# Kernel optimization log

Measured on AMD Instinct MI355X. Metric: run time of the kernel, lower is better.

Reference implementation:

```python
import jax, jax.numpy as jnp
import numpy as np

POS_MARGIN = 0.01
NEG_MARGIN = 0.2
REG_WEIGHT = 0.1
N, D = 8192, 256
NUM_CLASSES = 512


def setup_inputs() -> dict:
    key = jax.random.key(0)
    k1, k2 = jax.random.split(key)
    embeds = jax.random.normal(k1, (N, D), dtype=jnp.float32)
    labels = jax.random.randint(k2, (N,), 0, NUM_CLASSES, dtype=jnp.int64)
    return {"embeds": embeds, "labels": labels}


def reference(embeds, labels):
    n, d = embeds.shape
    # L2-normalize embeddings (normalize_embeds=True)
    e = embeds / jnp.linalg.norm(embeds, axis=1, keepdims=True)

    # var(e_i - e_j, ddof=1) over feature dim, computed without the [N,N,D] tensor:
    # var = (D/(D-1)) * ( mean(e_i^2) + mean(e_j^2) - 2*mean(e_i*e_j) - (m_i - m_j)^2 )
    m = e.mean(axis=1)                      # [N]
    s = (e * e).mean(axis=1)                # [N]
    g = (e @ e.T) / d                       # [N,N] = mean(e_i * e_j) over D
    corr = d / (d - 1.0)
    var_diff = corr * (s[:, None] + s[None, :] - 2.0 * g - (m[:, None] - m[None, :]) ** 2)
    row_var = corr * (s - m * m)            # torch.var(e, dim=1), unbiased
    distmat = var_diff / row_var[:, None]

    same = labels[:, None] == labels[None, :]
    eye = jnp.eye(n, dtype=bool)
    pos_mask = same & (~eye)                # all same-label pairs (anchor != positive)
    neg_mask = ~same                        # all diff-label pairs

    pos_l = jax.nn.relu(distmat - POS_MARGIN) * pos_mask
    neg_l = jax.nn.relu(NEG_MARGIN - distmat) * neg_mask

    # avg_nonzero_only=True: sum / (# strictly-positive entries + 1e-12)
    pos_loss = pos_l.sum() / ((pos_l > 0).sum().astype(jnp.float32) + 1e-12)
    neg_loss = neg_l.sum() / ((neg_l > 0).sum().astype(jnp.float32) + 1e-12)

    loss = pos_loss + neg_loss
    loss = loss + jnp.abs(e.sum(axis=1)).mean() * REG_WEIGHT
    return loss
```

## Files before the change

### kernel.cpp

```cpp
#include <hip/hip_runtime.h>

#define NROWS 8192
#define DDIM 256
#define BT 64
#define BK 64
#define GT (NROWS / BT)
#define NBT (GT * (GT + 1) / 2)

using bf16x8 = __attribute__((ext_vector_type(8))) __bf16;
using f32x4  = __attribute__((ext_vector_type(4))) float;

__device__ __forceinline__ void glds16(const unsigned short* g, unsigned short* l) {
    __builtin_amdgcn_global_load_lds(
        (const __attribute__((address_space(1))) unsigned int*)g,
        (__attribute__((address_space(3))) unsigned int*)l,
        16, 0, 0);
}

__device__ __forceinline__ unsigned short f2bf(float f) {
    unsigned int b = __float_as_uint(f);
    unsigned int r = b + 0x7fffu + ((b >> 16) & 1u);
    return (unsigned short)(r >> 16);
}

__global__ __launch_bounds__(256) void rowstats_kernel(
    const float* __restrict__ x, unsigned short* __restrict__ ebf,
    float* __restrict__ aP, float* __restrict__ bs,
    float* __restrict__ rabs)
{
    int wave = threadIdx.x >> 6;
    int lane = threadIdx.x & 63;
    int row  = blockIdx.x * 4 + wave;

    const float4 v = reinterpret_cast<const float4*>(x + (size_t)row * DDIM)[lane];
    float ss = v.x * v.x + v.y * v.y + v.z * v.z + v.w * v.w;
    float sm = v.x + v.y + v.z + v.w;
    #pragma unroll
    for (int off = 32; off >= 1; off >>= 1) {
        ss += __shfl_xor(ss, off);
        sm += __shfl_xor(sm, off);
    }
    float invn = 1.0f / sqrtf(ss);
    float m = sm * invn * (1.0f / DDIM);

    ushort4 o;
    o.x = f2bf(v.x * invn - m);
    o.y = f2bf(v.y * invn - m);
    o.z = f2bf(v.z * invn - m);
    o.w = f2bf(v.w * invn - m);
    reinterpret_cast<ushort4*>(ebf + (size_t)row * DDIM)[lane] = o;

    if (lane == 0) {
        float s  = ss * invn * invn * (1.0f / DDIM);
        float b  = s - m * m;
        float a  = 1.0f / b;
        aP[row]   = a * (1.0f / 128.0f);
        bs[row]   = -128.0f * b;
        rabs[row] = fabsf(sm * invn);
    }
}

__global__ __launch_bounds__(256, 8) void snr_gemm_kernel(
    const unsigned short* __restrict__ ebf,
    const float* __restrict__ aP, const float* __restrict__ bs,
    const int* __restrict__ labels,
    float* __restrict__ partials)
{
    __shared__ __align__(16) unsigned short As[BT * BK];
    __shared__ __align__(16) unsigned short Bs[BT * BK];
    __shared__ float sAPi[BT], sBsi[BT];
    __shared__ float sAPj[BT], sBsj[BT];
    __shared__ int   sLi[BT], sLj[BT];
    __shared__ float redbuf[4][4];

    int tid  = threadIdx.x;
    int lane = tid & 63;
    int wave = tid >> 6;
    int wr = (wave >> 1) * 32;
    int wc = (wave & 1) * 32;

    int t = blockIdx.x;
    int bi = (int)((2.0f * GT + 1.0f
                    - sqrtf((2.0f * GT + 1.0f) * (2.0f * GT + 1.0f) - 8.0f * (float)t)) * 0.5f);
    while ((bi + 1) * GT - ((bi + 1) * bi) / 2 <= t) ++bi;
    while (bi * GT - (bi * (bi - 1)) / 2 > t) --bi;
    int bj = bi + (t - (bi * GT - (bi * (bi - 1)) / 2));
    int rowBase = bi * BT, colBase = bj * BT;
    bool diag = (bi == bj);

    if (tid < BT) {
        int gi = rowBase + tid;
        sAPi[tid] = aP[gi]; sBsi[tid] = bs[gi];
        sLi[tid] = labels[gi];
    } else if (tid < 2 * BT) {
        int tt = tid - BT;
        int gj = colBase + tt;
        sAPj[tt] = aP[gj]; sBsj[tt] = bs[gj];
        sLj[tt] = labels[gj];
    }

    const unsigned short* gA[2];
    const unsigned short* gB[2];
    unsigned short* lpA[2];
    unsigned short* lpB[2];
    #pragma unroll
    for (int p = 0; p < 2; ++p) {
        int q   = p * 256 + tid;
        int row = q >> 3;
        int kc  = (q & 7) ^ (row & 7);
        gA[p] = ebf + (size_t)(rowBase + row) * DDIM + kc * 8;
        gB[p] = ebf + (size_t)(colBase + row) * DDIM + kc * 8;
        lpA[p] = As + q * 8;
        lpB[p] = Bs + q * 8;
    }

    int mrow = lane & 15;
    int kch  = lane >> 4;
    int offA[2][2], offB[2][2];
    #pragma unroll
    for (int t4 = 0; t4 < 2; ++t4) {
        int rA = wr + t4 * 16 + mrow;
        int rB = wc + t4 * 16 + mrow;
        #pragma unroll
        for (int h = 0; h < 2; ++h) {
            offA[t4][h] = (rA * 8 + ((h * 4 + kch) ^ (rA & 7))) * 8;
            offB[t4][h] = (rB * 8 + ((h * 4 + kch) ^ (rB & 7))) * 8;
        }
    }

    f32x4 acc[2][2];
    #pragma unroll
    for (int a = 0; a < 2; ++a)
        #pragma unroll
        for (int b = 0; b < 2; ++b)
            acc[a][b] = (f32x4){0.f, 0.f, 0.f, 0.f};

    for (int it = 0; it < 4; ++it) {
        #pragma unroll
        for (int p = 0; p < 2; ++p) {
            glds16(gA[p], lpA[p]);
            glds16(gB[p], lpB[p]);
            gA[p] += BK;
            gB[p] += BK;
        }
        asm volatile("s_waitcnt vmcnt(0)" ::: "memory");
        __syncthreads();

        #pragma unroll
        for (int h = 0; h < 2; ++h) {
            bf16x8 aF[2], bF[2];
            #pragma unroll
            for (int t4 = 0; t4 < 2; ++t4) {
                aF[t4] = *reinterpret_cast<const bf16x8*>(As + offA[t4][h]);
                bF[t4] = *reinterpret_cast<const bf16x8*>(Bs + offB[t4][h]);
            }
            #pragma unroll
            for (int ti = 0; ti < 2; ++ti)
                #pragma unroll
                for (int tj = 0; tj < 2; ++tj)
                    acc[ti][tj] = __builtin_amdgcn_mfma_f32_16x16x32_bf16(aF[ti], bF[tj], acc[ti][tj], 0, 0, 0);
        }
        __syncthreads();
    }

    int subr = (lane >> 4) * 4;
    int cj   = lane & 15;

    float aPC[2], bsC[2];
    int LCj[2];
    #pragma unroll
    for (int tj = 0; tj < 2; ++tj) {
        int lj = wc + tj * 16 + cj;
        aPC[tj] = sAPj[lj]; bsC[tj] = sBsj[lj];
        LCj[tj] = sLj[lj];
    }

    float Sn = 0.f, Sp = 0.f;
    unsigned Cn = 0u, Cp = 0u;

    if (!diag) {
        #pragma unroll
        for (int ti = 0; ti < 2; ++ti) {
            #pragma unroll
            for (int r = 0; r < 4; ++r) {
                int li = wr + ti * 16 + subr + r;
                float aR = sAPi[li], bR = sBsi[li];
                int LR = sLi[li];
                #pragma unroll
                for (int tj = 0; tj < 2; ++tj) {
                    float raw = acc[ti][tj][r];
                    float v1 = fmaf(aR, raw + bsC[tj], -0.8f);
                    float v2 = fmaf(aPC[tj], raw + bR, -0.8f);
                    bool same = (LR == LCj[tj]);
                    unsigned long long b1 = __ballot(v1 > 0.f);
                    unsigned long long b2 = __ballot(v2 > 0.f);
                    unsigned long long ms = __ballot(same);
                    if (b1 | b2 | ms) {
                        float nz = fmaxf(v1, 0.f) + fmaxf(v2, 0.f);
                        Sn += same ? 0.f : nz;
                        float pz = fmaxf(0.19f - v1, 0.f) + fmaxf(0.19f - v2, 0.f);
                        Sp += same ? pz : 0.f;
                        Cn += (unsigned)__popcll(b1 & ~ms)
                            + (unsigned)__popcll(b2 & ~ms);
                        Cp += (unsigned)__popcll(__ballot(v1 < 0.19f) & ms)
                            + (unsigned)__popcll(__ballot(v2 < 0.19f) & ms);
                    }
                }
            }
        }
    } else {
        #pragma unroll
        for (int ti = 0; ti < 2; ++ti) {
            #pragma unroll
            for (int r = 0; r < 4; ++r) {
                int li = wr + ti * 16 + subr + r;
                float aR = sAPi[li];
                int LR = sLi[li];
                #pragma unroll
                for (int tj = 0; tj < 2; ++tj) {
                    int lj = wc + tj * 16 + cj;
                    float raw = acc[ti][tj][r];
                    float v1 = fmaf(aR, raw + bsC[tj], -0.8f);
                    bool same = (LR == LCj[tj]);
                    bool pok  = same && (li != lj);
                    unsigned long long b1 = __ballot(v1 > 0.f);
                    unsigned long long ms = __ballot(same);
                    if (b1 | ms) {
                        unsigned long long mp = __ballot(pok);
                        Sn += same ? 0.f : fmaxf(v1, 0.f);
                        float pz = fmaxf(0.19f - v1, 0.f);
                        Sp += pok ? pz : 0.f;
                        Cn += (unsigned)__popcll(b1 & ~ms);
                        Cp += (unsigned)__popcll(__ballot(v1 < 0.19f) & mp);
                    }
                }
            }
        }
    }

    #pragma unroll
    for (int off = 32; off >= 1; off >>= 1) {
        Sn += __shfl_down(Sn, off);
        Sp += __shfl_down(Sp, off);
    }
    if (lane == 0) {
        redbuf[wave][0] = Sn; redbuf[wave][1] = (float)Cn;
        redbuf[wave][2] = Sp; redbuf[wave][3] = (float)Cp;
    }
    __syncthreads();
    if (tid < 4) {
        partials[blockIdx.x * 4 + tid] =
            redbuf[0][tid] + redbuf[1][tid] + redbuf[2][tid] + redbuf[3][tid];
    }
}

__global__ __launch_bounds__(256) void finalize_kernel(
    const float* __restrict__ partials, const float* __restrict__ rabs,
    float* __restrict__ out)
{
    int tid = threadIdx.x;
    float s0 = 0, s1 = 0, s2 = 0, s3 = 0, rr = 0;
    for (int i = tid; i < NBT; i += 256) {
        float4 p = reinterpret_cast<const float4*>(partials)[i];
        s0 += p.x; s1 += p.y; s2 += p.z; s3 += p.w;
    }
    for (int i = tid; i < NROWS; i += 256) rr += rabs[i];

    #pragma unroll
    for (int off = 32; off >= 1; off >>= 1) {
        s0 += __shfl_down(s0, off);
        s1 += __shfl_down(s1, off);
        s2 += __shfl_down(s2, off);
        s3 += __shfl_down(s3, off);
        rr += __shfl_down(rr, off);
    }
    __shared__ float red[4][5];
    int wave = tid >> 6, lane = tid & 63;
    if (lane == 0) {
        red[wave][0] = s0; red[wave][1] = s1; red[wave][2] = s2;
        red[wave][3] = s3; red[wave][4] = rr;
    }
    __syncthreads();
    if (tid == 0) {
        float a0 = 0, a1 = 0, a2 = 0, a3 = 0, a4 = 0;
        #pragma unroll
        for (int w = 0; w < 4; ++w) {
            a0 += red[w][0]; a1 += red[w][1]; a2 += red[w][2];
            a3 += red[w][3]; a4 += red[w][4];
        }
        float neg = (a1 > 0.5f) ? a0 / (a1 + 1e-12f) : 0.0f;
        float pos = (a3 > 0.5f) ? a2 / (a3 + 1e-12f) : 0.0f;
        out[0] = pos + neg + a4 * (0.1f / (float)NROWS);
    }
}

extern "C" void kernel_launch(void* const* d_in, const int* in_sizes, int n_in,
                              void* d_out, int out_size, void* d_ws, size_t ws_size,
                              hipStream_t stream) {
    const float* embeds = (const float*)d_in[0];
    const int*   labels = (const int*)d_in[1];
    float* out = (float*)d_out;

    char* ws = (char*)d_ws;
    unsigned short* ebf = (unsigned short*)ws;
    float* aP   = (float*)(ws + (size_t)NROWS * DDIM * 2);
    float* bs   = aP + NROWS;
    float* rabs = bs + NROWS;
    float* partials = rabs + NROWS;

    rowstats_kernel<<<NROWS / 4, 256, 0, stream>>>(embeds, ebf, aP, bs, rabs);

    snr_gemm_kernel<<<NBT, 256, 0, stream>>>(ebf, aP, bs, labels, partials);

    finalize_kernel<<<1, 256, 0, stream>>>(partials, rabs, out);
}
```

Before: 112.1 us.

## Fuse rowstats, GEMM loss and finalize into one persistent cooperative kernel

Replaces three kernel launches with a single cooperative persistent kernel. It computes row statistics, syncs the grid, loops over triangular tiles in a grid-stride loop, syncs again, and has block 0 finalize the loss. The aim is to remove launch overhead and tail effects between kernels. In exchange it adds two grid-wide barriers and limits the grid to resident blocks, and it loses the oversubscription that previously let the hardware balance tile work across CUs.

```diff
diff --git a/kernel.cpp b/kernel.cpp
--- a/kernel.cpp
+++ b/kernel.cpp
@@ -1,4 +1,7 @@
 #include <hip/hip_runtime.h>
+#include <hip/hip_cooperative_groups.h>
+
+namespace cg = cooperative_groups;
 
 #define NROWS 8192
 #define DDIM 256
@@ -23,99 +26,60 @@
     return (unsigned short)(r >> 16);
 }
 
-__global__ __launch_bounds__(256) void rowstats_kernel(
-    const float* __restrict__ x, unsigned short* __restrict__ ebf,
-    float* __restrict__ aP, float* __restrict__ bs,
-    float* __restrict__ rabs)
-{
-    int wave = threadIdx.x >> 6;
-    int lane = threadIdx.x & 63;
-    int row  = blockIdx.x * 4 + wave;
-
-    const float4 v = reinterpret_cast<const float4*>(x + (size_t)row * DDIM)[lane];
-    float ss = v.x * v.x + v.y * v.y + v.z * v.z + v.w * v.w;
-    float sm = v.x + v.y + v.z + v.w;
-    #pragma unroll
-    for (int off = 32; off >= 1; off >>= 1) {
-        ss += __shfl_xor(ss, off);
-        sm += __shfl_xor(sm, off);
-    }
-    float invn = 1.0f / sqrtf(ss);
-    float m = sm * invn * (1.0f / DDIM);
-
-    ushort4 o;
-    o.x = f2bf(v.x * invn - m);
-    o.y = f2bf(v.y * invn - m);
-    o.z = f2bf(v.z * invn - m);
-    o.w = f2bf(v.w * invn - m);
-    reinterpret_cast<ushort4*>(ebf + (size_t)row * DDIM)[lane] = o;
-
-    if (lane == 0) {
-        float s  = ss * invn * invn * (1.0f / DDIM);
-        float b  = s - m * m;
-        float a  = 1.0f / b;
-        aP[row]   = a * (1.0f / 128.0f);
-        bs[row]   = -128.0f * b;
-        rabs[row] = fabsf(sm * invn);
-    }
-}
-
-__global__ __launch_bounds__(256, 8) void snr_gemm_kernel(
-    const unsigned short* __restrict__ ebf,
-    const float* __restrict__ aP, const float* __restrict__ bs,
-    const int* __restrict__ labels,
-    float* __restrict__ partials)
+__global__ __launch_bounds__(256, 8) void snr_fused_kernel(
+    const float* __restrict__ x, const int* __restrict__ labels,
+    unsigned short* __restrict__ ebf, float* __restrict__ aP,
+    float* __restrict__ bsv, float* __restrict__ rabs,
+    float* __restrict__ partials, float* __restrict__ out)
 {
     __shared__ __align__(16) unsigned short As[BT * BK];
     __shared__ __align__(16) unsigned short Bs[BT * BK];
     __shared__ float sAPi[BT], sBsi[BT];
     __shared__ float sAPj[BT], sBsj[BT];
     __shared__ int   sLi[BT], sLj[BT];
-    __shared__ float redbuf[4][4];
+    __shared__ float redbuf[4][5];
 
     int tid  = threadIdx.x;
     int lane = tid & 63;
     int wave = tid >> 6;
+
+    for (int q = blockIdx.x; q < NROWS / 4; q += gridDim.x) {
+        int row = q * 4 + wave;
+        const float4 v = reinterpret_cast<const float4*>(x + (size_t)row * DDIM)[lane];
+        float ss = v.x * v.x + v.y * v.y + v.z * v.z + v.w * v.w;
+        float sm = v.x + v.y + v.z + v.w;
+        #pragma unroll
+        for (int off = 32; off >= 1; off >>= 1) {
+            ss += __shfl_xor(ss, off);
+            sm += __shfl_xor(sm, off);
+        }
+        float invn = 1.0f / sqrtf(ss);
+        float m = sm * invn * (1.0f / DDIM);
+
+        ushort4 o;
+        o.x = f2bf(v.x * invn - m);
+        o.y = f2bf(v.y * invn - m);
+        o.z = f2bf(v.z * invn - m);
+        o.w = f2bf(v.w * invn - m);
+        reinterpret_cast<ushort4*>(ebf + (size_t)row * DDIM)[lane] = o;
+
+        if (lane == 0) {
+            float s  = ss * invn * invn * (1.0f / DDIM);
+            float b  = s - m * m;
+            float a  = 1.0f / b;
+            aP[row]   = a * (1.0f / 128.0f);
+            bsv[row]  = -128.0f * b;
+            rabs[row] = fabsf(sm * invn);
+        }
+    }
+
+    cg::this_grid().sync();
+
     int wr = (wave >> 1) * 32;
     int wc = (wave & 1) * 32;
-
-    int t = blockIdx.x;
-    int bi = (int)((2.0f * GT + 1.0f
-                    - sqrtf((2.0f * GT + 1.0f) * (2.0f * GT + 1.0f) - 8.0f * (float)t)) * 0.5f);
-    while ((bi + 1) * GT - ((bi + 1) * bi) / 2 <= t) ++bi;
-    while (bi * GT - (bi * (bi - 1)) / 2 > t) --bi;
-    int bj = bi + (t - (bi * GT - (bi * (bi - 1)) / 2));
-    int rowBase = bi * BT, colBase = bj * BT;
-    bool diag = (bi == bj);
-
-    if (tid < BT) {
-        int gi = rowBase + tid;
-        sAPi[tid] = aP[gi]; sBsi[tid] = bs[gi];
-        sLi[tid] = labels[gi];
-    } else if (tid < 2 * BT) {
-        int tt = tid - BT;
-        int gj = colBase + tt;
-        sAPj[tt] = aP[gj]; sBsj[tt] = bs[gj];
-        sLj[tt] = labels[gj];
-    }
-
-    const unsigned short* gA[2];
-    const unsigned short* gB[2];
-    unsigned short* lpA[2];
-    unsigned short* lpB[2];
-    #pragma unroll
-    for (int p = 0; p < 2; ++p) {
-        int q   = p * 256 + tid;
-        int row = q >> 3;
-        int kc  = (q & 7) ^ (row & 7);
-        gA[p] = ebf + (size_t)(rowBase + row) * DDIM + kc * 8;
-        gB[p] = ebf + (size_t)(colBase + row) * DDIM + kc * 8;
-        lpA[p] = As + q * 8;
-        lpB[p] = Bs + q * 8;
-    }
-
     int mrow = lane & 15;
     int kch  = lane >> 4;
+
     int offA[2][2], offB[2][2];
     #pragma unroll
     for (int t4 = 0; t4 < 2; ++t4) {
@@ -127,115 +91,155 @@
             offB[t4][h] = (rB * 8 + ((h * 4 + kch) ^ (rB & 7))) * 8;
         }
     }
-
-    f32x4 acc[2][2];
+    unsigned short* lpA[2];
+    unsigned short* lpB[2];
+    int srow[2], skc[2];
     #pragma unroll
-    for (int a = 0; a < 2; ++a)
-        #pragma unroll
-        for (int b = 0; b < 2; ++b)
-            acc[a][b] = (f32x4){0.f, 0.f, 0.f, 0.f};
-
-    for (int it = 0; it < 4; ++it) {
-        #pragma unroll
-        for (int p = 0; p < 2; ++p) {
-            glds16(gA[p], lpA[p]);
-            glds16(gB[p], lpB[p]);
-            gA[p] += BK;
-            gB[p] += BK;
-        }
-        asm volatile("s_waitcnt vmcnt(0)" ::: "memory");
-        __syncthreads();
-
-        #pragma unroll
-        for (int h = 0; h < 2; ++h) {
-            bf16x8 aF[2], bF[2];
-            #pragma unroll
-            for (int t4 = 0; t4 < 2; ++t4) {
-                aF[t4] = *reinterpret_cast<const bf16x8*>(As + offA[t4][h]);
-                bF[t4] = *reinterpret_cast<const bf16x8*>(Bs + offB[t4][h]);
-            }
-            #pragma unroll
-            for (int ti = 0; ti < 2; ++ti)
-                #pragma unroll
-                for (int tj = 0; tj < 2; ++tj)
-                    acc[ti][tj] = __builtin_amdgcn_mfma_f32_16x16x32_bf16(aF[ti], bF[tj], acc[ti][tj], 0, 0, 0);
-        }
-        __syncthreads();
-    }
-
+    for (int p = 0; p < 2; ++p) {
+        int q = p * 256 + tid;
+        srow[p] = q >> 3;
+        skc[p]  = ((q & 7) ^ (srow[p] & 7)) * 8;
+        lpA[p] = As + q * 8;
+        lpB[p] = Bs + q * 8;
+    }
+
+    float Sn = 0.f, Sp = 0.f;
+    unsigned Cn = 0u, Cp = 0u;
     int subr = (lane >> 4) * 4;
     int cj   = lane & 15;
 
-    float aPC[2], bsC[2];
-    int LCj[2];
-    #pragma unroll
-    for (int tj = 0; tj < 2; ++tj) {
-        int lj = wc + tj * 16 + cj;
-        aPC[tj] = sAPj[lj]; bsC[tj] = sBsj[lj];
-        LCj[tj] = sLj[lj];
-    }
-
-    float Sn = 0.f, Sp = 0.f;
-    unsigned Cn = 0u, Cp = 0u;
-
-    if (!diag) {
-        #pragma unroll
-        for (int ti = 0; ti < 2; ++ti) {
-            #pragma unroll
-            for (int r = 0; r < 4; ++r) {
-                int li = wr + ti * 16 + subr + r;
-                float aR = sAPi[li], bR = sBsi[li];
-                int LR = sLi[li];
+    for (int t = blockIdx.x; t < NBT; t += gridDim.x) {
+        int bi = (int)((2.0f * GT + 1.0f
+                        - sqrtf((2.0f * GT + 1.0f) * (2.0f * GT + 1.0f) - 8.0f * (float)t)) * 0.5f);
+        while ((bi + 1) * GT - ((bi + 1) * bi) / 2 <= t) ++bi;
+        while (bi * GT - (bi * (bi - 1)) / 2 > t) --bi;
+        int bj = bi + (t - (bi * GT - (bi * (bi - 1)) / 2));
+        int rowBase = bi * BT, colBase = bj * BT;
+        bool diag = (bi == bj);
+
+        if (tid < BT) {
+            int gi = rowBase + tid;
+            sAPi[tid] = aP[gi]; sBsi[tid] = bsv[gi];
+            sLi[tid] = labels[gi];
+        } else if (tid < 2 * BT) {
+            int tt = tid - BT;
+            int gj = colBase + tt;
+            sAPj[tt] = aP[gj]; sBsj[tt] = bsv[gj];
+            sLj[tt] = labels[gj];
+        }
+
+        const unsigned short* gA[2];
+        const unsigned short* gB[2];
+        #pragma unroll
+        for (int p = 0; p < 2; ++p) {
+            gA[p] = ebf + (size_t)(rowBase + srow[p]) * DDIM + skc[p];
+            gB[p] = ebf + (size_t)(colBase + srow[p]) * DDIM + skc[p];
+        }
+
+        f32x4 acc[2][2];
+        #pragma unroll
+        for (int a = 0; a < 2; ++a)
+            #pragma unroll
+            for (int b = 0; b < 2; ++b)
+                acc[a][b] = (f32x4){0.f, 0.f, 0.f, 0.f};
+
+        for (int it = 0; it < 4; ++it) {
+            #pragma unroll
+            for (int p = 0; p < 2; ++p) {
+                glds16(gA[p], lpA[p]);
+                glds16(gB[p], lpB[p]);
+                gA[p] += BK;
+                gB[p] += BK;
+            }
+            asm volatile("s_waitcnt vmcnt(0)" ::: "memory");
+            __syncthreads();
+
+            #pragma unroll
+            for (int h = 0; h < 2; ++h) {
+                bf16x8 aF[2], bF[2];
                 #pragma unroll
-                for (int tj = 0; tj < 2; ++tj) {
-                    float raw = acc[ti][tj][r];
-                    float v1 = fmaf(aR, raw + bsC[tj], -0.8f);
-                    float v2 = fmaf(aPC[tj], raw + bR, -0.8f);
-                    bool same = (LR == LCj[tj]);
-                    unsigned long long b1 = __ballot(v1 > 0.f);
-                    unsigned long long b2 = __ballot(v2 > 0.f);
-                    unsigned long long ms = __ballot(same);
-                    if (b1 | b2 | ms) {
-                        float nz = fmaxf(v1, 0.f) + fmaxf(v2, 0.f);
-                        Sn += same ? 0.f : nz;
-                        float pz = fmaxf(0.19f - v1, 0.f) + fmaxf(0.19f - v2, 0.f);
-                        Sp += same ? pz : 0.f;
-                        Cn += (unsigned)__popcll(b1 & ~ms)
-                            + (unsigned)__popcll(b2 & ~ms);
-                        Cp += (unsigned)__popcll(__ballot(v1 < 0.19f) & ms)
-                            + (unsigned)__popcll(__ballot(v2 < 0.19f) & ms);
+                for (int t4 = 0; t4 < 2; ++t4) {
+                    aF[t4] = *reinterpret_cast<const bf16x8*>(As + offA[t4][h]);
+                    bF[t4] = *reinterpret_cast<const bf16x8*>(Bs + offB[t4][h]);
+                }
+                #pragma unroll
+                for (int ti = 0; ti < 2; ++ti)
+                    #pragma unroll
+                    for (int tj = 0; tj < 2; ++tj)
+                        acc[ti][tj] = __builtin_amdgcn_mfma_f32_16x16x32_bf16(aF[ti], bF[tj], acc[ti][tj], 0, 0, 0);
+            }
+            __syncthreads();
+        }
+
+        float aPC[2], bsC[2];
+        int LCj[2];
+        #pragma unroll
+        for (int tj = 0; tj < 2; ++tj) {
+            int lj = wc + tj * 16 + cj;
+            aPC[tj] = sAPj[lj]; bsC[tj] = sBsj[lj];
+            LCj[tj] = sLj[lj];
+        }
+
+        if (!diag) {
+            #pragma unroll
+            for (int ti = 0; ti < 2; ++ti) {
+                #pragma unroll
+                for (int r = 0; r < 4; ++r) {
+                    int li = wr + ti * 16 + subr + r;
+                    float aR = sAPi[li], bR = sBsi[li];
+                    int LR = sLi[li];
+                    #pragma unroll
+                    for (int tj = 0; tj < 2; ++tj) {
+                        float raw = acc[ti][tj][r];
+                        float v1 = fmaf(aR, raw + bsC[tj], -0.8f);
+                        float v2 = fmaf(aPC[tj], raw + bR, -0.8f);
+                        bool same = (LR == LCj[tj]);
+                        unsigned long long b1 = __ballot(v1 > 0.f);
+                        unsigned long long b2 = __ballot(v2 > 0.f);
+                        unsigned long long ms = __ballot(same);
+                        if (b1 | b2 | ms) {
+                            float nz = fmaxf(v1, 0.f) + fmaxf(v2, 0.f);
+                            Sn += same ? 0.f : nz;
+                            float pz = fmaxf(0.19f - v1, 0.f) + fmaxf(0.19f - v2, 0.f);
+                            Sp += same ? pz : 0.f;
+                            Cn += (unsigned)__popcll(b1 & ~ms)
+                                + (unsigned)__popcll(b2 & ~ms);
+                            Cp += (unsigned)__popcll(__ballot(v1 < 0.19f) & ms)
+                                + (unsigned)__popcll(__ballot(v2 < 0.19f) & ms);
+                        }
                     }
                 }
             }
-        }
-    } else {
-        #pragma unroll
-        for (int ti = 0; ti < 2; ++ti) {
-            #pragma unroll
-            for (int r = 0; r < 4; ++r) {
-                int li = wr + ti * 16 + subr + r;
-                float aR = sAPi[li];
-                int LR = sLi[li];
+        } else {
+            #pragma unroll
+            for (int ti = 0; ti < 2; ++ti) {
                 #pragma unroll
-                for (int tj = 0; tj < 2; ++tj) {
-                    int lj = wc + tj * 16 + cj;
-                    float raw = acc[ti][tj][r];
-                    float v1 = fmaf(aR, raw + bsC[tj], -0.8f);
-                    bool same = (LR == LCj[tj]);
-                    bool pok  = same && (li != lj);
-                    unsigned long long b1 = __ballot(v1 > 0.f);
-                    unsigned long long ms = __ballot(same);
-                    if (b1 | ms) {
-                        unsigned long long mp = __ballot(pok);
-                        Sn += same ? 0.f : fmaxf(v1, 0.f);
-                        float pz = fmaxf(0.19f - v1, 0.f);
-                        Sp += pok ? pz : 0.f;
-                        Cn += (unsigned)__popcll(b1 & ~ms);
-                        Cp += (unsigned)__popcll(__ballot(v1 < 0.19f) & mp);
+                for (int r = 0; r < 4; ++r) {
+                    int li = wr + ti * 16 + subr + r;
+                    float aR = sAPi[li];
+                    int LR = sLi[li];
+                    #pragma unroll
+                    for (int tj = 0; tj < 2; ++tj) {
+                        int lj = wc + tj * 16 + cj;
+                        float raw = acc[ti][tj][r];
+                        float v1 = fmaf(aR, raw + bsC[tj], -0.8f);
+                        bool same = (LR == LCj[tj]);
+                        bool pok  = same && (li != lj);
+                        unsigned long long b1 = __ballot(v1 > 0.f);
+                        unsigned long long ms = __ballot(same);
+                        if (b1 | ms) {
+                            unsigned long long mp = __ballot(pok);
+                            Sn += same ? 0.f : fmaxf(v1, 0.f);
+                            float pz = fmaxf(0.19f - v1, 0.f);
+                            Sp += pok ? pz : 0.f;
+                            Cn += (unsigned)__popcll(b1 & ~ms);
+                            Cp += (unsigned)__popcll(__ballot(v1 < 0.19f) & mp);
+                        }
                     }
                 }
             }
         }
+        __syncthreads();
     }
 
     #pragma unroll
@@ -252,45 +256,43 @@
         partials[blockIdx.x * 4 + tid] =
             redbuf[0][tid] + redbuf[1][tid] + redbuf[2][tid] + redbuf[3][tid];
     }
-}
-
-__global__ __launch_bounds__(256) void finalize_kernel(
-    const float* __restrict__ partials, const float* __restrict__ rabs,
-    float* __restrict__ out)
-{
-    int tid = threadIdx.x;
-    float s0 = 0, s1 = 0, s2 = 0, s3 = 0, rr = 0;
-    for (int i = tid; i < NBT; i += 256) {
-        float4 p = reinterpret_cast<const float4*>(partials)[i];
-        s0 += p.x; s1 += p.y; s2 += p.z; s3 += p.w;
-    }
-    for (int i = tid; i < NROWS; i += 256) rr += rabs[i];
-
-    #pragma unroll
-    for (int off = 32; off >= 1; off >>= 1) {
-        s0 += __shfl_down(s0, off);
-        s1 += __shfl_down(s1, off);
-        s2 += __shfl_down(s2, off);
-        s3 += __shfl_down(s3, off);
-        rr += __shfl_down(rr, off);
-    }
-    __shared__ float red[4][5];
-    int wave = tid >> 6, lane = tid & 63;
-    if (lane == 0) {
-        red[wave][0] = s0; red[wave][1] = s1; red[wave][2] = s2;
-        red[wave][3] = s3; red[wave][4] = rr;
-    }
-    __syncthreads();
-    if (tid == 0) {
-        float a0 = 0, a1 = 0, a2 = 0, a3 = 0, a4 = 0;
-        #pragma unroll
-        for (int w = 0; w < 4; ++w) {
-            a0 += red[w][0]; a1 += red[w][1]; a2 += red[w][2];
-            a3 += red[w][3]; a4 += red[w][4];
-        }
-        float neg = (a1 > 0.5f) ? a0 / (a1 + 1e-12f) : 0.0f;
-        float pos = (a3 > 0.5f) ? a2 / (a3 + 1e-12f) : 0.0f;
-        out[0] = pos + neg + a4 * (0.1f / (float)NROWS);
+
+    cg::this_grid().sync();
+
+    if (blockIdx.x == 0) {
+        float s0 = 0, s1 = 0, s2 = 0, s3 = 0, rr = 0;
+        int g = gridDim.x;
+        for (int i = tid; i < g; i += 256) {
+            float4 p = reinterpret_cast<const float4*>(partials)[i];
+            s0 += p.x; s1 += p.y; s2 += p.z; s3 += p.w;
+        }
+        for (int i = tid; i < NROWS; i += 256) rr += rabs[i];
+
+        #pragma unroll
+        for (int off = 32; off >= 1; off >>= 1) {
+            s0 += __shfl_down(s0, off);
+            s1 += __shfl_down(s1, off);
+            s2 += __shfl_down(s2, off);
+            s3 += __shfl_down(s3, off);
+            rr += __shfl_down(rr, off);
+        }
+        __syncthreads();
+        if (lane == 0) {
+            redbuf[wave][0] = s0; redbuf[wave][1] = s1; redbuf[wave][2] = s2;
+            redbuf[wave][3] = s3; redbuf[wave][4] = rr;
+        }
+        __syncthreads();
+        if (tid == 0) {
+            float a0 = 0, a1 = 0, a2 = 0, a3 = 0, a4 = 0;
+            #pragma unroll
+            for (int w = 0; w < 4; ++w) {
+                a0 += redbuf[w][0]; a1 += redbuf[w][1]; a2 += redbuf[w][2];
+                a3 += redbuf[w][3]; a4 += redbuf[w][4];
+            }
+            float neg = (a1 > 0.5f) ? a0 / (a1 + 1e-12f) : 0.0f;
+            float pos = (a3 > 0.5f) ? a2 / (a3 + 1e-12f) : 0.0f;
+            out[0] = pos + neg + a4 * (0.1f / (float)NROWS);
+        }
     }
 }
 
@@ -304,13 +306,24 @@
     char* ws = (char*)d_ws;
     unsigned short* ebf = (unsigned short*)ws;
     float* aP   = (float*)(ws + (size_t)NROWS * DDIM * 2);
-    float* bs   = aP + NROWS;
-    float* rabs = bs + NROWS;
+    float* bsv  = aP + NROWS;
+    float* rabs = bsv + NROWS;
     float* partials = rabs + NROWS;
 
-    rowstats_kernel<<<NROWS / 4, 256, 0, stream>>>(embeds, ebf, aP, bs, rabs);
-
-    snr_gemm_kernel<<<NBT, 256, 0, stream>>>(ebf, aP, bs, labels, partials);
-
-    finalize_kernel<<<1, 256, 0, stream>>>(partials, rabs, out);
+    static int gblocks = 0;
+    if (gblocks == 0) {
+        int per = 0;
+        if (hipOccupancyMaxActiveBlocksPerMultiprocessor(&per, snr_fused_kernel, 256, 0)
+                != hipSuccess || per < 1) per = 8;
+        if (per > 8) per = 8;
+        gblocks = per * 256;
+        if (gblocks > NROWS / 4) gblocks = NROWS / 4;
+    }
+
+    void* args[] = {
+        (void*)&embeds, (void*)&labels, (void*)&ebf, (void*)&aP,
+        (void*)&bsv, (void*)&rabs, (void*)&partials, (void*)&out
+    };
+    hipLaunchCooperativeKernel((void*)snr_fused_kernel, dim3(gblocks), dim3(256),
+                               args, 0, stream);
 }
```

Result: slower. 306.6 us (+173.5%).
